# Kernel tuning notes

Hardware: AMD Instinct MI355X
Metric: run time of the kernel (lower is better)

Reference implementation:

```python
import jax, jax.numpy as jnp
import numpy as np

N = 100000      # num nodes
E = 3200000     # num edges
F = 128         # feature dim (in == out, required by final in-place copy)
U = 1000        # num_users


def gcn_conv(x, edge_index, W, b):
    """PyG GCNConv: symmetric-normalized adjacency with self-loops.
    out = D^{-1/2} (A + I) D^{-1/2} X W + b
    """
    xw = x @ W                                   # [N, F]
    src, dst = edge_index[0], edge_index[1]
    # in-degree including the self-loop (+1)
    deg = jax.ops.segment_sum(jnp.ones((E,), x.dtype), dst, num_segments=N) + 1.0
    inv_sqrt = jax.lax.rsqrt(deg)                # [N]
    coef = inv_sqrt[src] * inv_sqrt[dst]         # [E]
    agg = jax.ops.segment_sum(xw[src] * coef[:, None], dst, num_segments=N)
    # self-loop contribution: norm_ii = inv_sqrt[i]^2
    return agg + xw * (inv_sqrt * inv_sqrt)[:, None] + b


def setup_inputs() -> dict:
    key = jax.random.key(0)
    k1, k2, k3, k4, k5, k6 = jax.random.split(key, 6)
    x = jax.random.normal(k1, (N, F), dtype=jnp.float32)
    edge_index = jax.random.randint(k2, (2, E), 0, N, dtype=jnp.int64)
    s = 1.0 / np.sqrt(F)
    W1 = jax.random.normal(k3, (F, F), dtype=jnp.float32) * s
    b1 = jnp.zeros((F,), dtype=jnp.float32)
    W2 = jax.random.normal(k4, (F, F), dtype=jnp.float32) * s
    b2 = jnp.zeros((F,), dtype=jnp.float32)
    return {"x": x, "edge_index": edge_index, "W1": W1, "b1": b1, "W2": W2, "b2": b2}


def reference(x, edge_index, W1, b1, W2, b2):
    # eval mode: dropout(p=0.5, training=False) is identity; detach is a no-op in fwd
    h = jax.nn.elu(gcn_conv(x, edge_index, W1, b1))
    h = jax.nn.elu(gcn_conv(h, edge_index, W2, b2))
    # x[num_users:] = movie_features  -> movie rows restored to original input
    return jnp.concatenate([h[:U], x[U:]], axis=0)
```

## Files before the change

kernel.cpp:

```cpp
#include <hip/hip_runtime.h>


#define F_DIM 128
#define U_USERS 1000
#define SCAN_CHUNK 1024
#define NFCAP 48000
#define NCHUNK 3
#define SBIN 40960
#define SW (SBIN / 2)
#define PSLICE 85
#define XPAD 136
#define BMW 3136

using f16x8 = __attribute__((ext_vector_type(8))) _Float16;
using f16x2 = __attribute__((ext_vector_type(2))) _Float16;
using f32x4 = __attribute__((ext_vector_type(4))) float;

union H4 { uint2 u2; _Float16 h[4]; };

__global__ __launch_bounds__(1024) void hist_kernel(const int* __restrict__ src,
                                                    const int* __restrict__ dst,
                                                    unsigned int* __restrict__ partial,
                                                    int* __restrict__ fr, int E, int n) {
    __shared__ unsigned int h[SW];
    int tid = threadIdx.x;
    int c = blockIdx.x % NCHUNK;
    int p = blockIdx.x / NCHUNK;
    for (int i = tid; i < SW; i += 1024) h[i] = 0u;
    __syncthreads();

    int lo = c * SBIN;
    int hi = lo + SBIN;
    int len = (E + PSLICE - 1) / PSLICE;
    int base = p * len;
    int end = min(E, base + len);
    int e = base + tid * 4;
    for (; e + 3 < end; e += 4096) {
        int4 dv = *(const int4*)(dst + e);
#pragma unroll
        for (int i = 0; i < 4; ++i) {
            int d = ((const int*)&dv)[i];
            if ((unsigned)d < (unsigned)n) {
                if (d >= lo && d < hi) {
                    int local = d - lo;
                    atomicAdd(&h[local >> 1], 1u << ((local & 1) << 4));
                }
                if (c == 0 && d < U_USERS) {
                    int s = src[e + i];
                    if ((unsigned)s < (unsigned)n) fr[s] = 1;
                }
            }
        }
    }
    for (; e < end; ++e) {
        int d = dst[e];
        if ((unsigned)d < (unsigned)n) {
            if (d >= lo && d < hi) {
                int local = d - lo;
                atomicAdd(&h[local >> 1], 1u << ((local & 1) << 4));
            }
            if (c == 0 && d < U_USERS) {
                int s = src[e];
                if ((unsigned)s < (unsigned)n) fr[s] = 1;
            }
        }
    }
    __syncthreads();
    unsigned int* outp = partial + ((size_t)(c * PSLICE + p)) * SW;
    for (int i = tid; i < SW; i += 1024) outp[i] = h[i];
}

__global__ void reduce_prep_kernel(const unsigned int* __restrict__ partial,
                                   float* __restrict__ inv, int* __restrict__ fr,
                                   int* __restrict__ degF,
                                   unsigned int* __restrict__ bitsG, int n) {
    int t = blockIdx.x * blockDim.x + threadIdx.x;
    if (t >= NCHUNK * SW) return;
    int c = t / SW, w = t % SW;
    unsigned int a0 = 0, a1 = 0;
    const unsigned int* basep = partial + (size_t)c * PSLICE * SW + w;
#pragma unroll 5
    for (int p = 0; p < PSLICE; ++p) {
        unsigned int v = basep[(size_t)p * SW];
        a0 += v & 0xFFFFu;
        a1 += v >> 16;
    }
    int i0 = c * SBIN + 2 * w;
    unsigned int pair = 0u;
#pragma unroll
    for (int k = 0; k < 2; ++k) {
        int i = i0 + k;
        unsigned int dg = k ? a1 : a0;
        if (i < n) {
            inv[i] = rsqrtf((float)dg + 1.0f);
            bool isfr = (i < U_USERS) || (fr[i] != 0);
            if (i < U_USERS) fr[i] = 1;
            degF[i] = isfr ? (int)dg : 0;
            if (isfr) pair |= (1u << k);
        }
    }
    if (pair) atomicOr(&bitsG[i0 >> 5], pair << (i0 & 31));
}

__global__ void scan_reduce2_kernel(const int* __restrict__ dA, const int* __restrict__ dB,
                                    int* __restrict__ pA, int* __restrict__ pB, int n) {
    __shared__ int sdata[256];
    int b = blockIdx.x, t = threadIdx.x;
    int base = b * SCAN_CHUNK;
    int sumA = 0, sumB = 0;
#pragma unroll
    for (int i = 0; i < 4; ++i) {
        int idx = base + t + 256 * i;
        if (idx < n) { sumA += dA[idx]; sumB += dB[idx]; }
    }
    sdata[t] = sumA; __syncthreads();
    for (int s = 128; s > 0; s >>= 1) { if (t < s) sdata[t] += sdata[t + s]; __syncthreads(); }
    if (t == 0) pA[b] = sdata[0];
    __syncthreads();
    sdata[t] = sumB; __syncthreads();
    for (int s = 128; s > 0; s >>= 1) { if (t < s) sdata[t] += sdata[t + s]; __syncthreads(); }
    if (t == 0) pB[b] = sdata[0];
}

__global__ void scan_partials2_kernel(int* __restrict__ pA, int* __restrict__ pB, int nb) {
    int wv = threadIdx.x >> 6, lane = threadIdx.x & 63;
    int* p = wv ? pB : pA;
    int i0 = lane * 2, i1 = lane * 2 + 1;
    int v0 = (i0 < nb) ? p[i0] : 0;
    int v1 = (i1 < nb) ? p[i1] : 0;
    int sum = v0 + v1;
    int incl = sum;
    for (int ofs = 1; ofs < 64; ofs <<= 1) {
        int t = __shfl_up(incl, ofs);
        if (lane >= ofs) incl += t;
    }
    int run = incl - sum;
    if (i0 < nb) p[i0] = run;
    if (i1 < nb) p[i1] = run + v0;
}

__global__ void scan_final2_kernel(const int* __restrict__ dA, const int* __restrict__ pA,
                                   int* __restrict__ rp,
                                   const int* __restrict__ dB, const int* __restrict__ pB,
                                   int* __restrict__ remap,
                                   int* __restrict__ flist, int* __restrict__ nf_dev, int n) {
    __shared__ int sthread[256];
    int b = blockIdx.x, t = threadIdx.x;
    int base = b * SCAN_CHUNK;
    {
        int v[4]; int sum = 0;
#pragma unroll
        for (int i = 0; i < 4; ++i) { int idx = base + 4 * t + i; v[i] = (idx < n) ? dA[idx] : 0; sum += v[i]; }
        sthread[t] = sum; __syncthreads();
        for (int ofs = 1; ofs < 256; ofs <<= 1) {
            int val = (t >= ofs) ? sthread[t - ofs] : 0;
            __syncthreads(); sthread[t] += val; __syncthreads();
        }
        int run = sthread[t] - sum + pA[b];
#pragma unroll
        for (int i = 0; i < 4; ++i) { int idx = base + 4 * t + i; if (idx < n) rp[idx] = run; run += v[i]; }
        __syncthreads();
    }
    {
        int v[4]; int sum = 0;
#pragma unroll
        for (int i = 0; i < 4; ++i) { int idx = base + 4 * t + i; v[i] = (idx < n) ? dB[idx] : 0; sum += v[i]; }
        sthread[t] = sum; __syncthreads();
        for (int ofs = 1; ofs < 256; ofs <<= 1) {
            int val = (t >= ofs) ? sthread[t - ofs] : 0;
            __syncthreads(); sthread[t] += val; __syncthreads();
        }
        int run = sthread[t] - sum + pB[b];
#pragma unroll
        for (int i = 0; i < 4; ++i) {
            int idx = base + 4 * t + i;
            if (idx < n) {
                remap[idx] = run;
                if (v[i] && run < NFCAP) flist[run] = idx;
                if (idx == n - 1) *nf_dev = min(run + v[i], NFCAP);
            }
            run += v[i];
        }
    }
}

__global__ __launch_bounds__(256) void fill_csr_kernel(const int* __restrict__ src,
                                                       const int* __restrict__ dst,
                                                       const unsigned int* __restrict__ bitsG,
                                                       int* __restrict__ rp, int* __restrict__ col,
                                                       int E, int n) {
    __shared__ unsigned int bm[BMW];
    int tid = threadIdx.x;
    int nw = (n + 31) >> 5;
    for (int i = tid; i < nw; i += 256) bm[i] = bitsG[i];
    __syncthreads();

    int t = blockIdx.x * 256 + tid;
    int e0 = t * 4;
    if (e0 + 3 < E) {
        int4 dv = *(const int4*)(dst + e0);
        int4 sv = *(const int4*)(src + e0);
        const int* dp = (const int*)&dv;
        const int* sp = (const int*)&sv;
        bool f[4];
#pragma unroll
        for (int i = 0; i < 4; ++i) {
            int d = dp[i];
            f[i] = ((unsigned)d < (unsigned)n) && ((unsigned)sp[i] < (unsigned)n)
                   && ((bm[d >> 5] >> (d & 31)) & 1u);
        }
        int pos[4];
#pragma unroll
        for (int i = 0; i < 4; ++i) {
            pos[i] = -1;
            if (f[i]) pos[i] = atomicAdd(&rp[dp[i]], 1);
        }
#pragma unroll
        for (int i = 0; i < 4; ++i) {
            if (f[i] && (unsigned)pos[i] < (unsigned)E) col[pos[i]] = sp[i];
        }
    } else {
        for (int e = e0; e < E; ++e) {
            int d = dst[e], s = src[e];
            if ((unsigned)d < (unsigned)n && (unsigned)s < (unsigned)n &&
                ((bm[d >> 5] >> (d & 31)) & 1u)) {
                int pos = atomicAdd(&rp[d], 1);
                if ((unsigned)pos < (unsigned)E) col[pos] = s;
            }
        }
    }
}

__device__ __forceinline__ void gemm_mfma_body(const float* __restrict__ X,
                                               const float* __restrict__ W,
                                               _Float16* __restrict__ outh,
                                               float* __restrict__ pout,
                                               int nrows, int rowBase) {
    __shared__ _Float16 Wt[128 * XPAD];
    __shared__ _Float16 Xs[64 * XPAD];

    int tid = threadIdx.x;

    const float4* W4 = (const float4*)W;
#pragma unroll
    for (int i = 0; i < 16; ++i) {
        int j = tid + 256 * i;
        int k = j >> 5;
        int n4 = j & 31;
        float4 v = W4[j];
#pragma unroll
        for (int q = 0; q < 4; ++q)
            Wt[(n4 * 4 + q) * XPAD + k] = (_Float16)((const float*)&v)[q];
    }

#pragma unroll
    for (int i = 0; i < 8; ++i) {
        int j = tid + 256 * i;
        int r = j >> 5;
        int k4 = j & 31;
        int row = rowBase + r;
        float4 v = make_float4(0.f, 0.f, 0.f, 0.f);
        if (row < nrows) {
            v = ((const float4*)(X + (size_t)row * F_DIM))[k4];
            if (pout != nullptr && row >= U_USERS)
                ((float4*)(pout + (size_t)row * F_DIM))[k4] = v;
        }
        H4 p;
#pragma unroll
        for (int q = 0; q < 4; ++q) p.h[q] = (_Float16)((const float*)&v)[q];
        *(uint2*)&Xs[r * XPAD + k4 * 4] = p.u2;
    }
    __syncthreads();

    int w = tid >> 6;
    int lane = tid & 63;
    int m = lane & 15;
    int quad = lane >> 4;
    int R = w * 16;

    f32x4 acc[8];
#pragma unroll
    for (int i = 0; i < 8; ++i) acc[i] = (f32x4){0.f, 0.f, 0.f, 0.f};

#pragma unroll
    for (int kc = 0; kc < 4; ++kc) {
        f16x8 a = *(const f16x8*)&Xs[(R + m) * XPAD + kc * 32 + quad * 8];
#pragma unroll
        for (int ct = 0; ct < 8; ++ct) {
            f16x8 b = *(const f16x8*)&Wt[(ct * 16 + m) * XPAD + kc * 32 + quad * 8];
            acc[ct] = __builtin_amdgcn_mfma_f32_16x16x32_f16(a, b, acc[ct], 0, 0, 0);
        }
    }

#pragma unroll
    for (int ct = 0; ct < 8; ++ct) {
#pragma unroll
        for (int reg = 0; reg < 4; ++reg) {
            int row = rowBase + R + quad * 4 + reg;
            if (row < nrows)
                outh[(size_t)row * F_DIM + ct * 16 + m] = (_Float16)acc[ct][reg];
        }
    }
}

__global__ __launch_bounds__(256) void gemm_f16_kernel(const float* __restrict__ X,
                                                       const float* __restrict__ W,
                                                       _Float16* __restrict__ outh,
                                                       float* __restrict__ pout, int nrows) {
    gemm_mfma_body(X, W, outh, pout, nrows, blockIdx.x * 64);
}

__global__ __launch_bounds__(256) void gemm_f16_dyn_kernel(const float* __restrict__ X,
                                                           const float* __restrict__ W,
                                                           _Float16* __restrict__ outh,
                                                           const int* __restrict__ nrows_p) {
    int nrows = *nrows_p;
    int rowBase = blockIdx.x * 64;
    if (rowBase >= nrows) return;
    gemm_mfma_body(X, W, outh, nullptr, nrows, rowBase);
}

__global__ __launch_bounds__(256) void gather_l1_kernel(const _Float16* __restrict__ xwh,
                                                        const float* __restrict__ inv,
                                                        const int* __restrict__ rp,
                                                        const int* __restrict__ col,
                                                        const int* __restrict__ flist,
                                                        const int* __restrict__ nf_p,
                                                        const float* __restrict__ b,
                                                        float* __restrict__ h1c) {
    int ci = blockIdx.x * 4 + (threadIdx.x >> 6);
    if (ci >= *nf_p) return;
    int lane = threadIdx.x & 63;
    int node = flist[ci];
    int start = (node == 0) ? 0 : rp[node - 1];
    int end = rp[node];

    float accx = 0.f, accy = 0.f;
    for (int base = start; base < end; base += 64) {
        int j = base + lane;
        int s_l = 0; float c_l = 0.f;
        if (j < end) { s_l = col[j]; c_l = inv[s_l]; }
        int cnt = min(64, end - base);
        int i = 0;
        for (; i + 4 <= cnt; i += 4) {
            int s0 = __shfl(s_l, i + 0); float f0 = __shfl(c_l, i + 0);
            int s1 = __shfl(s_l, i + 1); float f1 = __shfl(c_l, i + 1);
            int s2 = __shfl(s_l, i + 2); float f2 = __shfl(c_l, i + 2);
            int s3 = __shfl(s_l, i + 3); float f3 = __shfl(c_l, i + 3);
            f16x2 v0 = ((const f16x2*)(xwh + (size_t)s0 * F_DIM))[lane];
            f16x2 v1 = ((const f16x2*)(xwh + (size_t)s1 * F_DIM))[lane];
            f16x2 v2 = ((const f16x2*)(xwh + (size_t)s2 * F_DIM))[lane];
            f16x2 v3 = ((const f16x2*)(xwh + (size_t)s3 * F_DIM))[lane];
            accx += (float)v0[0] * f0 + (float)v1[0] * f1 + (float)v2[0] * f2 + (float)v3[0] * f3;
            accy += (float)v0[1] * f0 + (float)v1[1] * f1 + (float)v2[1] * f2 + (float)v3[1] * f3;
        }
        for (; i < cnt; ++i) {
            int s0 = __shfl(s_l, i); float f0 = __shfl(c_l, i);
            f16x2 v0 = ((const f16x2*)(xwh + (size_t)s0 * F_DIM))[lane];
            accx += (float)v0[0] * f0;
            accy += (float)v0[1] * f0;
        }
    }

    float ivd = inv[node];
    f16x2 self = ((const f16x2*)(xwh + (size_t)node * F_DIM))[lane];
    float vx = accx * ivd + (float)self[0] * ivd * ivd + b[lane * 2];
    float vy = accy * ivd + (float)self[1] * ivd * ivd + b[lane * 2 + 1];
    vx = vx > 0.f ? vx : expf(vx) - 1.f;
    vy = vy > 0.f ? vy : expf(vy) - 1.f;
    ((float2*)(h1c + (size_t)ci * F_DIM))[lane] = make_float2(vx, vy);
}

__global__ __launch_bounds__(256) void gather_l2_kernel(const _Float16* __restrict__ xwc,
                                                        const float* __restrict__ inv,
                                                        const int* __restrict__ rp,
                                                        const int* __restrict__ col,
                                                        const int* __restrict__ remap,
                                                        const float* __restrict__ b,
                                                        float* __restrict__ out) {
    int node = blockIdx.x * 4 + (threadIdx.x >> 6);
    if (node >= U_USERS) return;
    int lane = threadIdx.x & 63;
    int start = (node == 0) ? 0 : rp[node - 1];
    int end = rp[node];

    float accx = 0.f, accy = 0.f;
    for (int base = start; base < end; base += 64) {
        int j = base + lane;
        int r_l = 0; float c_l = 0.f;
        if (j < end) { int s = col[j]; c_l = inv[s]; r_l = remap[s]; }
        int cnt = min(64, end - base);
        int i = 0;
        for (; i + 4 <= cnt; i += 4) {
            int r0 = __shfl(r_l, i + 0); float f0 = __shfl(c_l, i + 0);
            int r1 = __shfl(r_l, i + 1); float f1 = __shfl(c_l, i + 1);
            int r2 = __shfl(r_l, i + 2); float f2 = __shfl(c_l, i + 2);
            int r3 = __shfl(r_l, i + 3); float f3 = __shfl(c_l, i + 3);
            f16x2 v0 = ((const f16x2*)(xwc + (size_t)r0 * F_DIM))[lane];
            f16x2 v1 = ((const f16x2*)(xwc + (size_t)r1 * F_DIM))[lane];
            f16x2 v2 = ((const f16x2*)(xwc + (size_t)r2 * F_DIM))[lane];
            f16x2 v3 = ((const f16x2*)(xwc + (size_t)r3 * F_DIM))[lane];
            accx += (float)v0[0] * f0 + (float)v1[0] * f1 + (float)v2[0] * f2 + (float)v3[0] * f3;
            accy += (float)v0[1] * f0 + (float)v1[1] * f1 + (float)v2[1] * f2 + (float)v3[1] * f3;
        }
        for (; i < cnt; ++i) {
            int rr = __shfl(r_l, i); float f0 = __shfl(c_l, i);
            f16x2 v0 = ((const f16x2*)(xwc + (size_t)rr * F_DIM))[lane];
            accx += (float)v0[0] * f0;
            accy += (float)v0[1] * f0;
        }
    }

    float ivd = inv[node];
    f16x2 self = ((const f16x2*)(xwc + (size_t)node * F_DIM))[lane];
    float vx = accx * ivd + (float)self[0] * ivd * ivd + b[lane * 2];
    float vy = accy * ivd + (float)self[1] * ivd * ivd + b[lane * 2 + 1];
    vx = vx > 0.f ? vx : expf(vx) - 1.f;
    vy = vy > 0.f ? vy : expf(vy) - 1.f;
    ((float2*)(out + (size_t)node * F_DIM))[lane] = make_float2(vx, vy);
}

extern "C" void kernel_launch(void* const* d_in, const int* in_sizes, int n_in,
                              void* d_out, int out_size, void* d_ws, size_t ws_size,
                              hipStream_t stream) {
    const float* x  = (const float*)d_in[0];
    const int*   ei = (const int*)d_in[1];
    const float* W1 = (const float*)d_in[2];
    const float* b1 = (const float*)d_in[3];
    const float* W2 = (const float*)d_in[4];
    const float* b2 = (const float*)d_in[5];
    float* out = (float*)d_out;

    int n = in_sizes[0] / F_DIM;
    int E = in_sizes[1] / 2;
    const int* srcI = ei;
    const int* dstI = ei + E;

    _Float16* xwh = (_Float16*)d_ws;
    float* h1c   = (float*)(xwh + (size_t)n * F_DIM);
    float* inv   = h1c + (size_t)NFCAP * F_DIM;
    int* fr      = (int*)(inv + n);
    int* degF    = fr + n;
    int* remap   = degF + n;
    int* rp      = remap + n;
    int* flist   = rp + n;
    int* pA      = flist + NFCAP;
    int* pB      = pA + 1024;
    int* nf_dev  = pB + 1024;
    int* col     = nf_dev + 16;
    unsigned int* partialH = (unsigned int*)(col + E);
    unsigned int* bitsG = partialH + (size_t)NCHUNK * PSLICE * SW;

    int nb = (n + SCAN_CHUNK - 1) / SCAN_CHUNK;

    hipMemsetAsync(fr, 0, (size_t)n * sizeof(int), stream);
    hipMemsetAsync(bitsG, 0, (size_t)BMW * sizeof(unsigned int), stream);

    hist_kernel<<<NCHUNK * PSLICE, 1024, 0, stream>>>(srcI, dstI, partialH, fr, E, n);
    reduce_prep_kernel<<<(NCHUNK * SW + 255) / 256, 256, 0, stream>>>(partialH, inv, fr, degF, bitsG, n);

    scan_reduce2_kernel<<<nb, 256, 0, stream>>>(degF, fr, pA, pB, n);
    scan_partials2_kernel<<<1, 128, 0, stream>>>(pA, pB, nb);
    scan_final2_kernel<<<nb, 256, 0, stream>>>(degF, pA, rp, fr, pB, remap, flist, nf_dev, n);

    fill_csr_kernel<<<(E / 4 + 255) / 256, 256, 0, stream>>>(srcI, dstI, bitsG, rp, col, E, n);

    gemm_f16_kernel<<<(n + 63) / 64, 256, 0, stream>>>(x, W1, xwh, out, n);
    gather_l1_kernel<<<(NFCAP + 3) / 4, 256, 0, stream>>>(xwh, inv, rp, col, flist, nf_dev, b1, h1c);

    gemm_f16_dyn_kernel<<<(NFCAP + 63) / 64, 256, 0, stream>>>(h1c, W2, xwh, nf_dev);
    gather_l2_kernel<<<(U_USERS + 3) / 4, 256, 0, stream>>>(xwh, inv, rp, col, remap, b2, out);
}
```

Before: 308.8 us.

## Merge CSR fill and layer-1 GEMM into one heterogeneous launch

Combines the independent fill_csr and layer-1 GEMM kernels into a single grid whose first blocks run the GEMM and whose remaining blocks fill the CSR, sharing one static shared-memory buffer. The aim is to overlap the atomic-heavy, memory-bound CSR fill with the MFMA GEMM and to save one launch boundary. In exchange, the fill blocks now reserve the GEMM's larger shared-memory footprint, which can lower how many of them fit on a compute unit at once.

Measured after the change: 299.1 us. 1.03x faster.

```diff
diff --git a/kernel.cpp b/kernel.cpp
--- a/kernel.cpp
+++ b/kernel.cpp
@@ -11,6 +11,7 @@
 #define PSLICE 85
 #define XPAD 136
 #define BMW 3136
+#define SMEM_BYTES (128 * XPAD * 2 + 64 * XPAD * 2)
 
 using f16x8 = __attribute__((ext_vector_type(8))) _Float16;
 using f16x2 = __attribute__((ext_vector_type(2))) _Float16;
@@ -184,18 +185,19 @@
     }
 }
 
-__global__ __launch_bounds__(256) void fill_csr_kernel(const int* __restrict__ src,
-                                                       const int* __restrict__ dst,
-                                                       const unsigned int* __restrict__ bitsG,
-                                                       int* __restrict__ rp, int* __restrict__ col,
-                                                       int E, int n) {
-    __shared__ unsigned int bm[BMW];
+__device__ __forceinline__ void fill_csr_body(const int* __restrict__ src,
+                                              const int* __restrict__ dst,
+                                              const unsigned int* __restrict__ bitsG,
+                                              int* __restrict__ rp, int* __restrict__ col,
+                                              int E, int n, int fblk,
+                                              unsigned char* smem) {
+    unsigned int* bm = (unsigned int*)smem;
     int tid = threadIdx.x;
     int nw = (n + 31) >> 5;
     for (int i = tid; i < nw; i += 256) bm[i] = bitsG[i];
     __syncthreads();
 
-    int t = blockIdx.x * 256 + tid;
+    int t = fblk * 256 + tid;
     int e0 = t * 4;
     if (e0 + 3 < E) {
         int4 dv = *(const int4*)(dst + e0);
@@ -235,9 +237,10 @@
                                                const float* __restrict__ W,
                                                _Float16* __restrict__ outh,
                                                float* __restrict__ pout,
-                                               int nrows, int rowBase) {
-    __shared__ _Float16 Wt[128 * XPAD];
-    __shared__ _Float16 Xs[64 * XPAD];
+                                               int nrows, int rowBase,
+                                               unsigned char* smem) {
+    _Float16* Wt = (_Float16*)smem;
+    _Float16* Xs = Wt + 128 * XPAD;
 
     int tid = threadIdx.x;
 
@@ -303,21 +306,34 @@
     }
 }
 
-__global__ __launch_bounds__(256) void gemm_f16_kernel(const float* __restrict__ X,
-                                                       const float* __restrict__ W,
-                                                       _Float16* __restrict__ outh,
-                                                       float* __restrict__ pout, int nrows) {
-    gemm_mfma_body(X, W, outh, pout, nrows, blockIdx.x * 64);
+__global__ __launch_bounds__(256) void gemm_fill_kernel(const float* __restrict__ X,
+                                                        const float* __restrict__ W,
+                                                        _Float16* __restrict__ outh,
+                                                        float* __restrict__ pout, int nrows,
+                                                        int gemmBlocks,
+                                                        const int* __restrict__ src,
+                                                        const int* __restrict__ dst,
+                                                        const unsigned int* __restrict__ bitsG,
+                                                        int* __restrict__ rp,
+                                                        int* __restrict__ col, int E, int n) {
+    __shared__ __align__(16) unsigned char smem[SMEM_BYTES];
+    int b = blockIdx.x;
+    if (b < gemmBlocks) {
+        gemm_mfma_body(X, W, outh, pout, nrows, b * 64, smem);
+    } else {
+        fill_csr_body(src, dst, bitsG, rp, col, E, n, b - gemmBlocks, smem);
+    }
 }
 
 __global__ __launch_bounds__(256) void gemm_f16_dyn_kernel(const float* __restrict__ X,
                                                            const float* __restrict__ W,
                                                            _Float16* __restrict__ outh,
                                                            const int* __restrict__ nrows_p) {
+    __shared__ __align__(16) unsigned char smem[SMEM_BYTES];
     int nrows = *nrows_p;
     int rowBase = blockIdx.x * 64;
     if (rowBase >= nrows) return;
-    gemm_mfma_body(X, W, outh, nullptr, nrows, rowBase);
+    gemm_mfma_body(X, W, outh, nullptr, nrows, rowBase, smem);
 }
 
 __global__ __launch_bounds__(256) void gather_l1_kernel(const _Float16* __restrict__ xwh,
@@ -463,9 +479,11 @@
     scan_partials2_kernel<<<1, 128, 0, stream>>>(pA, pB, nb);
     scan_final2_kernel<<<nb, 256, 0, stream>>>(degF, pA, rp, fr, pB, remap, flist, nf_dev, n);
 
-    fill_csr_kernel<<<(E / 4 + 255) / 256, 256, 0, stream>>>(srcI, dstI, bitsG, rp, col, E, n);
-
-    gemm_f16_kernel<<<(n + 63) / 64, 256, 0, stream>>>(x, W1, xwh, out, n);
+    int gemmBlocks = (n + 63) / 64;
+    int fillBlocks = (E / 4 + 255) / 256;
+    gemm_fill_kernel<<<gemmBlocks + fillBlocks, 256, 0, stream>>>(
+        x, W1, xwh, out, n, gemmBlocks, srcI, dstI, bitsG, rp, col, E, n);
+
     gather_l1_kernel<<<(NFCAP + 3) / 4, 256, 0, stream>>>(xwh, inv, rp, col, flist, nf_dev, b1, h1c);
 
     gemm_f16_dyn_kernel<<<(NFCAP + 63) / 64, 256, 0, stream>>>(h1c, W2, xwh, nf_dev);
```
